# Optimization experiments

Measured on AMD Instinct MI355X. Metric: run time of the kernel, lower is better.

## Reference

```python
import jax, jax.numpy as jnp
import numpy as np

DIM = 2048
NUM_HEADS = 16
NUM_KV_HEADS = 4
HEAD_DIM = DIM // NUM_HEADS  # 128


def apply_rotary_emb(x, freqs_cis):
    # x: [b, s, h, head_dim]; freqs_cis: [s, head_dim//2, 2]
    b, s, h, d = x.shape
    xs = x.reshape(b, s, h, d // 2, 2)
    fc = freqs_cis.reshape(1, s, 1, d // 2, 2)
    real = xs[..., 0] * fc[..., 0] - xs[..., 1] * fc[..., 1]
    imag = xs[..., 1] * fc[..., 0] + xs[..., 0] * fc[..., 1]
    return jnp.stack([real, imag], axis=-1).reshape(b, s, h, d)


def setup_inputs() -> dict:
    key = jax.random.key(0)
    k1, k2, k3, k4 = jax.random.split(key, 4)
    b, s = 2, 2048
    x = jax.random.normal(k1, (b, s, DIM), dtype=jnp.float32)
    freqs_cis = jax.random.uniform(k2, (s, HEAD_DIM // 2, 2), dtype=jnp.float32)
    total_kv_dim = (NUM_HEADS + 2 * NUM_KV_HEADS) * HEAD_DIM  # 3072
    wqkv = jax.random.normal(k3, (total_kv_dim, DIM), dtype=jnp.float32) * (DIM ** -0.5)
    wo = jax.random.normal(k4, (DIM, DIM), dtype=jnp.float32) * (DIM ** -0.5)
    return {"x": x, "freqs_cis": freqs_cis, "wqkv": wqkv, "wo": wo}


def reference(x, freqs_cis, wqkv, wo):
    b, s, _ = x.shape
    kv_size = NUM_KV_HEADS * HEAD_DIM
    qkv = jnp.einsum('bsd,od->bso', x, wqkv)
    xq = qkv[..., :DIM].reshape(b, s, NUM_HEADS, HEAD_DIM)
    xk = qkv[..., DIM:DIM + kv_size].reshape(b, s, NUM_KV_HEADS, HEAD_DIM)
    xv = qkv[..., DIM + kv_size:].reshape(b, s, NUM_KV_HEADS, HEAD_DIM)
    xq = apply_rotary_emb(xq, freqs_cis)
    xk = apply_rotary_emb(xk, freqs_cis)
    # -> [b, h, s, d]
    q = xq.transpose(0, 2, 1, 3)
    k = xk.transpose(0, 2, 1, 3)
    v = xv.transpose(0, 2, 1, 3)
    rep = NUM_HEADS // NUM_KV_HEADS
    k = jnp.repeat(k, rep, axis=1)
    v = jnp.repeat(v, rep, axis=1)
    scale = HEAD_DIM ** -0.5
    scores = jnp.einsum('bhqd,bhkd->bhqk', q, k) * scale
    causal = jnp.tril(jnp.ones((s, s), dtype=bool))
    scores = jnp.where(causal[None, None], scores, jnp.finfo(scores.dtype).min)
    attn = jax.nn.softmax(scores, axis=-1)
    out = jnp.einsum('bhqk,bhkd->bhqd', attn, v)
    out = out.transpose(0, 2, 1, 3).reshape(b, s, DIM)
    return jnp.einsum('bsd,od->bso', out, wo)
```

## Files before the change

### kernel.cpp

```cpp
#include <hip/hip_runtime.h>
#include <stdint.h>

typedef uint16_t u16;
typedef float f32x4 __attribute__((ext_vector_type(4)));
typedef short bf16x8 __attribute__((ext_vector_type(8)));

constexpr int NB = 2, NS = 2048, ND = 2048, NH = 16, NKVH = 4, HDIM = 128;
constexpr int QKVD = 3072;
constexpr int TOK = NB * NS;
constexpr float SM_SCALE = 0.08838834764831845f;
constexpr float LOG2E = 1.4426950408889634f;
constexpr float QK_SCALE = SM_SCALE * LOG2E;

#define WAITVM(N) asm volatile("s_waitcnt vmcnt(" #N ")" ::: "memory")
#define WAITLGKM0 asm volatile("s_waitcnt lgkmcnt(0)" ::: "memory")
#define MEMFENCE asm volatile("" ::: "memory")

__device__ __forceinline__ u16 f2bf(float f) {
  union { float f; uint32_t u; } v; v.f = f;
  return (u16)((v.u + 0x7fffu + ((v.u >> 16) & 1u)) >> 16);
}
__device__ __forceinline__ uint32_t cvt_pk_bf16(float lo, float hi) {
  uint32_t r;
  asm("v_cvt_pk_bf16_f32 %0, %1, %2" : "=v"(r) : "v"(lo), "v"(hi));
  return r;
}

__device__ __forceinline__ void gload_lds16(const void* g, void* l) {
  void* gv = const_cast<void*>(g);
  __builtin_amdgcn_global_load_lds(
      (__attribute__((address_space(1))) void*)gv,
      (__attribute__((address_space(3))) void*)l, 16, 0, 0);
}

__global__ __launch_bounds__(256) void cvt_bf16(const float* __restrict__ src,
                                                u16* __restrict__ dst, int n4) {
  int i = blockIdx.x * 256 + threadIdx.x;
  if (i >= n4) return;
  const float4 v = reinterpret_cast<const float4*>(src)[i];
  union { u16 h[4]; uint2 u; } o;
  o.h[0] = f2bf(v.x); o.h[1] = f2bf(v.y); o.h[2] = f2bf(v.z); o.h[3] = f2bf(v.w);
  reinterpret_cast<uint2*>(dst)[i] = o.u;
}

template <int MODE>
__global__ __launch_bounds__(256, 2)
void gemm_bt(const u16* __restrict__ A, const u16* __restrict__ Bm,
             void* __restrict__ Cv, int M, int N, int K,
             const float* __restrict__ fc, u16* __restrict__ Qb,
             u16* __restrict__ Kb, u16* __restrict__ Vt) {
  __shared__ u16 As[2][128 * 32];
  __shared__ u16 Bs[2][128 * 32];
  const int tid = threadIdx.x;
  const int lane = tid & 63;
  const int wid = tid >> 6;
  const int wr = wid >> 1, wc = wid & 1;
  const int rowA0 = blockIdx.y * 128, colB0 = blockIdx.x * 128;
  const int lr = lane & 15;
  const int lg = lane >> 4;
  const int lk = lg * 8;
  const char* Ab = (const char*)A;
  const char* Bb = (const char*)Bm;
  f32x4 acc[4][4] = {};
  const int nkt = K >> 5;

  auto STAGE = [&](int kt, int buf) {
#pragma unroll
    for (int p = 0; p < 2; ++p) {
      int o = p * 4096 + tid * 16;
      int row = o >> 6, kb = o & 63;
      gload_lds16(Ab + ((size_t)(rowA0 + row) * K + kt * 32) * 2 + kb, (char*)As[buf] + o);
      gload_lds16(Bb + ((size_t)(colB0 + row) * K + kt * 32) * 2 + kb, (char*)Bs[buf] + o);
    }
  };

  STAGE(0, 0);
  for (int kt = 0; kt < nkt; ++kt) {
    const int cur = kt & 1;
    if (kt + 1 < nkt) { STAGE(kt + 1, cur ^ 1); WAITVM(4); }
    else              { WAITVM(0); }
    __builtin_amdgcn_s_barrier();
    MEMFENCE;
    const u16* Ac = As[cur];
    const u16* Bc = Bs[cur];
    bf16x8 af[4], bfr[4];
#pragma unroll
    for (int m = 0; m < 4; ++m)
      af[m] = *(const bf16x8*)&Ac[(wr * 64 + m * 16 + lr) * 32 + lk];
#pragma unroll
    for (int n = 0; n < 4; ++n)
      bfr[n] = *(const bf16x8*)&Bc[(wc * 64 + n * 16 + lr) * 32 + lk];
    __builtin_amdgcn_s_setprio(1);
#pragma unroll
    for (int m = 0; m < 4; ++m)
#pragma unroll
      for (int n = 0; n < 4; ++n)
        acc[m][n] = __builtin_amdgcn_mfma_f32_16x16x32_bf16(af[m], bfr[n], acc[m][n], 0, 0, 0);
    __builtin_amdgcn_s_setprio(0);
    WAITLGKM0;
    __builtin_amdgcn_s_barrier();
    MEMFENCE;
  }

  if (MODE == 0) {
#pragma unroll
    for (int m = 0; m < 4; ++m) {
      int row0 = rowA0 + wr * 64 + m * 16 + lg * 4;
#pragma unroll
      for (int n = 0; n < 4; ++n) {
        int col = colB0 + wc * 64 + n * 16 + lr;
#pragma unroll
        for (int r = 0; r < 4; ++r)
          ((float*)Cv)[(size_t)(row0 + r) * N + col] = acc[m][n][r];
      }
    }
  } else {
    const int colblk = colB0 >> 7;
#pragma unroll
    for (int m = 0; m < 4; ++m) {
      int row0 = rowA0 + wr * 64 + m * 16 + lg * 4;
      int b_ = row0 >> 11;
      int s0 = row0 & 2047;
#pragma unroll
      for (int n = 0; n < 4; ++n) {
        int d = wc * 64 + n * 16 + lr;
        f32x4 v = acc[m][n];
        if (colblk < 20) {
          f32x4 pw;
#pragma unroll
          for (int r = 0; r < 4; ++r) pw[r] = __shfl_xor(v[r], 1, 64);
          int p = d >> 1;
          const bool ev = !(d & 1);
#pragma unroll
          for (int r = 0; r < 4; ++r) {
            int st = s0 + r;
            float c = fc[(st * 64 + p) * 2];
            float sn = fc[(st * 64 + p) * 2 + 1];
            float res = ev ? (v[r] * c - pw[r] * sn) : (v[r] * c + pw[r] * sn);
            if (colblk < 16)
              Qb[((size_t)(b_ * NH + colblk) * NS + st) * HDIM + d] = f2bf(res);
            else
              Kb[((size_t)(b_ * NKVH + (colblk - 16)) * NS + st) * HDIM + d] =
                  f2bf(res * QK_SCALE);
          }
        } else {
          int kv = colblk - 20;
          union { u16 h[4]; uint2 u; } o;
#pragma unroll
          for (int r = 0; r < 4; ++r) o.h[r] = f2bf(v[r]);
          *(uint2*)&Vt[((size_t)(b_ * NKVH + kv) * HDIM + d) * NS + s0] = o.u;
        }
      }
    }
  }
}

__global__ __launch_bounds__(512, 2)
void flash_attn(const u16* __restrict__ Qb, const u16* __restrict__ Kb,
                const u16* __restrict__ Vt, u16* __restrict__ Ob) {
  __shared__ u16 Ks[2][64 * 128];
  __shared__ u16 Vs[2][128 * 64];
  const int idx = blockIdx.x;
  const int grp = idx & 7;
  const int b = grp >> 2, kvh = grp & 3;
  const int rest = idx >> 3;
  const int h = kvh * 4 + (rest & 3);
  const int qt = (NS / 128 - 1) - (rest >> 2);
  const int tid = threadIdx.x, lane = tid & 63, w = tid >> 6;
  const int lr = lane & 15, lg = lane >> 4;

  bf16x8 aq[4];
  {
    const u16* Qrow = Qb + ((size_t)(b * NH + h) * NS + qt * 128 + w * 16 + lr) * HDIM;
#pragma unroll
    for (int ks = 0; ks < 4; ++ks)
      aq[ks] = *(const bf16x8*)(Qrow + ks * 32 + lg * 8);
  }
  bf16x8 ones;
#pragma unroll
  for (int j = 0; j < 8; ++j) ones[j] = (short)0x3F80;

  float mrun = -1e30f;
  f32x4 accl = {0.f, 0.f, 0.f, 0.f};
  f32x4 acco[8] = {};

  const char* Kbase = (const char*)(Kb + (size_t)(b * NKVH + kvh) * NS * HDIM);
  const char* Vbase = (const char*)(Vt + (size_t)(b * NKVH + kvh) * HDIM * NS);
  const int qglob = qt * 128 + w * 16 + lr;
  const int qrow0 = qt * 128 + w * 16 + lg * 4;
  const int wave_min_row = qt * 128 + w * 16;
  const int wave_max_row = wave_min_row + 15;

  auto STAGE = [&](int kt, int buf) {
#pragma unroll
    for (int p = 0; p < 2; ++p) {
      int o = p * 8192 + tid * 16;
      int krow = o >> 8, kwb = o & 255;
      gload_lds16(Kbase + (size_t)(kt * 64 + krow) * 256 + (kwb ^ ((krow & 7) << 4)),
                  (char*)Ks[buf] + o);
      int vrow = o >> 7, vwb = o & 127;
      gload_lds16(Vbase + (size_t)vrow * (NS * 2) + kt * 128 + (vwb ^ ((vrow & 7) << 4)),
                  (char*)Vs[buf] + o);
    }
  };

  const int ktmax = 2 * qt + 1;
  STAGE(0, 0);
  for (int kt = 0; kt <= ktmax; ++kt) {
    const int cur = kt & 1;
    if (kt < ktmax) { STAGE(kt + 1, cur ^ 1); WAITVM(4); }
    else            { WAITVM(0); }
    __builtin_amdgcn_s_barrier();
    MEMFENCE;

    if (kt * 64 <= wave_max_row) {
      const char* Kc = (const char*)Ks[cur];
      const char* Vc = (const char*)Vs[cur];

      f32x4 accs[4] = {};
      __builtin_amdgcn_s_setprio(1);
#pragma unroll
      for (int n = 0; n < 4; ++n) {
        int row = n * 16 + lr;
        int swz = (row & 7) << 4;
#pragma unroll
        for (int ks = 0; ks < 4; ++ks) {
          int cb = (ks * 32 + lg * 8) * 2;
          bf16x8 bk = *(const bf16x8*)(Kc + row * 256 + (cb ^ swz));
          accs[n] = __builtin_amdgcn_mfma_f32_16x16x32_bf16(bk, aq[ks], accs[n], 0, 0, 0);
        }
      }
      __builtin_amdgcn_s_setprio(0);

      if (kt * 64 + 63 > wave_min_row) {
#pragma unroll
        for (int n = 0; n < 4; ++n) {
          int kbase = kt * 64 + n * 16 + lg * 4;
#pragma unroll
          for (int r = 0; r < 4; ++r)
            if (kbase + r > qglob) accs[n][r] = -1e30f;
        }
      }

      float pmax = fmaxf(fmaxf(fmaxf(accs[0][0], accs[0][1]), fmaxf(accs[0][2], accs[0][3])),
                         fmaxf(fmaxf(accs[1][0], accs[1][1]), fmaxf(accs[1][2], accs[1][3])));
      pmax = fmaxf(pmax,
             fmaxf(fmaxf(fmaxf(accs[2][0], accs[2][1]), fmaxf(accs[2][2], accs[2][3])),
                   fmaxf(fmaxf(accs[3][0], accs[3][1]), fmaxf(accs[3][2], accs[3][3]))));
      pmax = fmaxf(pmax, __shfl_xor(pmax, 16, 64));
      pmax = fmaxf(pmax, __shfl_xor(pmax, 32, 64));

      bool ok = (pmax <= mrun + 8.f);
      if (!__all(ok)) {
        float mnew = fmaxf(mrun, pmax);
        float alpha = exp2f(mrun - mnew);
        mrun = mnew;
        float alr[4];
#pragma unroll
        for (int r = 0; r < 4; ++r)
          alr[r] = __shfl(alpha, lg * 4 + r, 64);
#pragma unroll
        for (int r = 0; r < 4; ++r) accl[r] *= alr[r];
#pragma unroll
        for (int n2 = 0; n2 < 8; ++n2)
#pragma unroll
          for (int r = 0; r < 4; ++r) acco[n2][r] *= alr[r];
      }

      uint32_t w0[4], w1[4];
#pragma unroll
      for (int n = 0; n < 4; ++n) {
        float p0 = exp2f(accs[n][0] - mrun);
        float p1 = exp2f(accs[n][1] - mrun);
        float p2 = exp2f(accs[n][2] - mrun);
        float p3 = exp2f(accs[n][3] - mrun);
        w0[n] = cvt_pk_bf16(p0, p1);
        w1[n] = cvt_pk_bf16(p2, p3);
      }

      const int s1 = ((lg & 1) << 5) | lr;
      const int s2 = s1 + 16;
      uint32_t F[4][4];
#pragma unroll
      for (int n = 0; n < 4; ++n) {
        F[n][0] = __shfl((int)w0[n], s1, 64);
        F[n][1] = __shfl((int)w1[n], s1, 64);
        F[n][2] = __shfl((int)w0[n], s2, 64);
        F[n][3] = __shfl((int)w1[n], s2, 64);
      }
      const bool hi = (lg & 2);
      bf16x8 pa[2];
#pragma unroll
      for (int ks = 0; ks < 2; ++ks) {
        union { uint32_t d[4]; bf16x8 v; } u;
#pragma unroll
        for (int j = 0; j < 4; ++j)
          u.d[j] = hi ? F[ks * 2 + 1][j] : F[ks * 2][j];
        pa[ks] = u.v;
      }

      __builtin_amdgcn_s_setprio(1);
#pragma unroll
      for (int ks = 0; ks < 2; ++ks) {
        int cb = (ks * 32 + lg * 8) * 2;
#pragma unroll
        for (int n2 = 0; n2 < 8; ++n2) {
          int d = n2 * 16 + lr;
          bf16x8 bv = *(const bf16x8*)(Vc + d * 128 + (cb ^ ((d & 7) << 4)));
          acco[n2] = __builtin_amdgcn_mfma_f32_16x16x32_bf16(pa[ks], bv, acco[n2], 0, 0, 0);
        }
        accl = __builtin_amdgcn_mfma_f32_16x16x32_bf16(pa[ks], ones, accl, 0, 0, 0);
      }
      __builtin_amdgcn_s_setprio(0);
    }
    WAITLGKM0;
    __builtin_amdgcn_s_barrier();
    MEMFENCE;
  }

#pragma unroll
  for (int n2 = 0; n2 < 8; ++n2) {
    int d = n2 * 16 + lr;
#pragma unroll
    for (int r = 0; r < 4; ++r) {
      int q = qrow0 + r;
      Ob[((size_t)b * NS + q) * ND + h * HDIM + d] = f2bf(acco[n2][r] / accl[r]);
    }
  }
}

extern "C" void kernel_launch(void* const* d_in, const int* in_sizes, int n_in,
                              void* d_out, int out_size, void* d_ws, size_t ws_size,
                              hipStream_t stream) {
  const float* x = (const float*)d_in[0];
  const float* fc = (const float*)d_in[1];
  const float* wqkv = (const float*)d_in[2];
  const float* wo = (const float*)d_in[3];
  float* out = (float*)d_out;
  char* ws = (char*)d_ws;
  size_t off = 0;
  u16* xb = (u16*)(ws + off);    off += (size_t)TOK * ND * 2;
  u16* wqkvb = (u16*)(ws + off); off += (size_t)QKVD * ND * 2;
  u16* wob = (u16*)(ws + off);   off += (size_t)ND * ND * 2;
  u16* Qb = (u16*)(ws + off);    off += (size_t)NB * NH * NS * HDIM * 2;
  u16* Kb = (u16*)(ws + off);    off += (size_t)NB * NKVH * NS * HDIM * 2;
  u16* Vtb = (u16*)(ws + off);   off += (size_t)NB * NKVH * NS * HDIM * 2;
  u16* attnb = (u16*)(ws + off); off += (size_t)TOK * ND * 2;
  (void)ws_size; (void)in_sizes; (void)n_in; (void)out_size;

  cvt_bf16<<<TOK * ND / 4 / 256, 256, 0, stream>>>(x, xb, TOK * ND / 4);
  cvt_bf16<<<QKVD * ND / 4 / 256, 256, 0, stream>>>(wqkv, wqkvb, QKVD * ND / 4);
  cvt_bf16<<<ND * ND / 4 / 256, 256, 0, stream>>>(wo, wob, ND * ND / 4);
  gemm_bt<2><<<dim3(QKVD / 128, TOK / 128), 256, 0, stream>>>(
      xb, wqkvb, nullptr, TOK, QKVD, ND, fc, Qb, Kb, Vtb);
  flash_attn<<<dim3(NB * NKVH * (NH / NKVH) * (NS / 128)), 512, 0, stream>>>(Qb, Kb, Vtb, attnb);
  gemm_bt<0><<<dim3(ND / 128, TOK / 128), 256, 0, stream>>>(
      attnb, wob, out, TOK, ND, ND, nullptr, nullptr, nullptr, nullptr);
}
```

Measured before the change: 220.1 us.

## Give each flash-attention wave two 16-row query chunks, halving block size

The flash attention kernel now runs 4 waves of 256 threads, each covering 32 query rows as two 16-row chunks, instead of 8 waves covering 16 rows each. Every K and V fragment read from LDS now feeds two MFMAs, so LDS read traffic per FLOP is halved. Each thread now issues 4 global-to-LDS loads per stage instead of 2, and the wait count is adjusted to match. The cost is about twice the accumulator registers per wave and fewer waves per block, which may lower occupancy and latency hiding. The causal-mask wave skip is also coarser, since it now works on 32 rows.

```diff
diff --git a/kernel.cpp b/kernel.cpp
--- a/kernel.cpp
+++ b/kernel.cpp
@@ -155,7 +155,7 @@
   }
 }
 
-__global__ __launch_bounds__(512, 2)
+__global__ __launch_bounds__(256, 2)
 void flash_attn(const u16* __restrict__ Qb, const u16* __restrict__ Kb,
                 const u16* __restrict__ Vt, u16* __restrict__ Ob) {
   __shared__ u16 Ks[2][64 * 128];
@@ -169,32 +169,31 @@
   const int tid = threadIdx.x, lane = tid & 63, w = tid >> 6;
   const int lr = lane & 15, lg = lane >> 4;
 
-  bf16x8 aq[4];
-  {
-    const u16* Qrow = Qb + ((size_t)(b * NH + h) * NS + qt * 128 + w * 16 + lr) * HDIM;
+  const int wr0 = qt * 128 + w * 32;
+
+  bf16x8 aq[2][4];
+#pragma unroll
+  for (int c = 0; c < 2; ++c) {
+    const u16* Qrow = Qb + ((size_t)(b * NH + h) * NS + wr0 + c * 16 + lr) * HDIM;
 #pragma unroll
     for (int ks = 0; ks < 4; ++ks)
-      aq[ks] = *(const bf16x8*)(Qrow + ks * 32 + lg * 8);
+      aq[c][ks] = *(const bf16x8*)(Qrow + ks * 32 + lg * 8);
   }
   bf16x8 ones;
 #pragma unroll
   for (int j = 0; j < 8; ++j) ones[j] = (short)0x3F80;
 
-  float mrun = -1e30f;
-  f32x4 accl = {0.f, 0.f, 0.f, 0.f};
-  f32x4 acco[8] = {};
+  float mrun[2] = {-1e30f, -1e30f};
+  f32x4 accl[2] = {};
+  f32x4 acco[2][8] = {};
 
   const char* Kbase = (const char*)(Kb + (size_t)(b * NKVH + kvh) * NS * HDIM);
   const char* Vbase = (const char*)(Vt + (size_t)(b * NKVH + kvh) * HDIM * NS);
-  const int qglob = qt * 128 + w * 16 + lr;
-  const int qrow0 = qt * 128 + w * 16 + lg * 4;
-  const int wave_min_row = qt * 128 + w * 16;
-  const int wave_max_row = wave_min_row + 15;
 
   auto STAGE = [&](int kt, int buf) {
 #pragma unroll
-    for (int p = 0; p < 2; ++p) {
-      int o = p * 8192 + tid * 16;
+    for (int p = 0; p < 4; ++p) {
+      int o = p * 4096 + tid * 16;
       int krow = o >> 8, kwb = o & 255;
       gload_lds16(Kbase + (size_t)(kt * 64 + krow) * 256 + (kwb ^ ((krow & 7) << 4)),
                   (char*)Ks[buf] + o);
@@ -208,16 +207,16 @@
   STAGE(0, 0);
   for (int kt = 0; kt <= ktmax; ++kt) {
     const int cur = kt & 1;
-    if (kt < ktmax) { STAGE(kt + 1, cur ^ 1); WAITVM(4); }
+    if (kt < ktmax) { STAGE(kt + 1, cur ^ 1); WAITVM(8); }
     else            { WAITVM(0); }
     __builtin_amdgcn_s_barrier();
     MEMFENCE;
 
-    if (kt * 64 <= wave_max_row) {
+    if (kt * 64 <= wr0 + 31) {
       const char* Kc = (const char*)Ks[cur];
       const char* Vc = (const char*)Vs[cur];
 
-      f32x4 accs[4] = {};
+      f32x4 accs[2][4] = {};
       __builtin_amdgcn_s_setprio(1);
 #pragma unroll
       for (int n = 0; n < 4; ++n) {
@@ -227,76 +226,82 @@
         for (int ks = 0; ks < 4; ++ks) {
           int cb = (ks * 32 + lg * 8) * 2;
           bf16x8 bk = *(const bf16x8*)(Kc + row * 256 + (cb ^ swz));
-          accs[n] = __builtin_amdgcn_mfma_f32_16x16x32_bf16(bk, aq[ks], accs[n], 0, 0, 0);
+          accs[0][n] = __builtin_amdgcn_mfma_f32_16x16x32_bf16(bk, aq[0][ks], accs[0][n], 0, 0, 0);
+          accs[1][n] = __builtin_amdgcn_mfma_f32_16x16x32_bf16(bk, aq[1][ks], accs[1][n], 0, 0, 0);
         }
       }
       __builtin_amdgcn_s_setprio(0);
 
-      if (kt * 64 + 63 > wave_min_row) {
+      bf16x8 pa[2][2];
+#pragma unroll
+      for (int c = 0; c < 2; ++c) {
+        const int cmin = wr0 + c * 16;
+        const int qg = cmin + lr;
+        if (kt * 64 + 63 > cmin) {
+#pragma unroll
+          for (int n = 0; n < 4; ++n) {
+            int kbase = kt * 64 + n * 16 + lg * 4;
+#pragma unroll
+            for (int r = 0; r < 4; ++r)
+              if (kbase + r > qg) accs[c][n][r] = -1e30f;
+          }
+        }
+
+        float pmax = fmaxf(
+            fmaxf(fmaxf(fmaxf(accs[c][0][0], accs[c][0][1]), fmaxf(accs[c][0][2], accs[c][0][3])),
+                  fmaxf(fmaxf(accs[c][1][0], accs[c][1][1]), fmaxf(accs[c][1][2], accs[c][1][3]))),
+            fmaxf(fmaxf(fmaxf(accs[c][2][0], accs[c][2][1]), fmaxf(accs[c][2][2], accs[c][2][3])),
+                  fmaxf(fmaxf(accs[c][3][0], accs[c][3][1]), fmaxf(accs[c][3][2], accs[c][3][3]))));
+        pmax = fmaxf(pmax, __shfl_xor(pmax, 16, 64));
+        pmax = fmaxf(pmax, __shfl_xor(pmax, 32, 64));
+
+        bool ok = (pmax <= mrun[c] + 8.f);
+        if (!__all(ok)) {
+          float mnew = fmaxf(mrun[c], pmax);
+          float alpha = exp2f(mrun[c] - mnew);
+          mrun[c] = mnew;
+          float alr[4];
+#pragma unroll
+          for (int r = 0; r < 4; ++r)
+            alr[r] = __shfl(alpha, lg * 4 + r, 64);
+#pragma unroll
+          for (int r = 0; r < 4; ++r) accl[c][r] *= alr[r];
+#pragma unroll
+          for (int n2 = 0; n2 < 8; ++n2)
+#pragma unroll
+            for (int r = 0; r < 4; ++r) acco[c][n2][r] *= alr[r];
+        }
+
+        uint32_t w0[4], w1[4];
 #pragma unroll
         for (int n = 0; n < 4; ++n) {
-          int kbase = kt * 64 + n * 16 + lg * 4;
-#pragma unroll
-          for (int r = 0; r < 4; ++r)
-            if (kbase + r > qglob) accs[n][r] = -1e30f;
-        }
-      }
-
-      float pmax = fmaxf(fmaxf(fmaxf(accs[0][0], accs[0][1]), fmaxf(accs[0][2], accs[0][3])),
-                         fmaxf(fmaxf(accs[1][0], accs[1][1]), fmaxf(accs[1][2], accs[1][3])));
-      pmax = fmaxf(pmax,
-             fmaxf(fmaxf(fmaxf(accs[2][0], accs[2][1]), fmaxf(accs[2][2], accs[2][3])),
-                   fmaxf(fmaxf(accs[3][0], accs[3][1]), fmaxf(accs[3][2], accs[3][3]))));
-      pmax = fmaxf(pmax, __shfl_xor(pmax, 16, 64));
-      pmax = fmaxf(pmax, __shfl_xor(pmax, 32, 64));
-
-      bool ok = (pmax <= mrun + 8.f);
-      if (!__all(ok)) {
-        float mnew = fmaxf(mrun, pmax);
-        float alpha = exp2f(mrun - mnew);
-        mrun = mnew;
-        float alr[4];
-#pragma unroll
-        for (int r = 0; r < 4; ++r)
-          alr[r] = __shfl(alpha, lg * 4 + r, 64);
-#pragma unroll
-        for (int r = 0; r < 4; ++r) accl[r] *= alr[r];
-#pragma unroll
-        for (int n2 = 0; n2 < 8; ++n2)
-#pragma unroll
-          for (int r = 0; r < 4; ++r) acco[n2][r] *= alr[r];
-      }
-
-      uint32_t w0[4], w1[4];
-#pragma unroll
-      for (int n = 0; n < 4; ++n) {
-        float p0 = exp2f(accs[n][0] - mrun);
-        float p1 = exp2f(accs[n][1] - mrun);
-        float p2 = exp2f(accs[n][2] - mrun);
-        float p3 = exp2f(accs[n][3] - mrun);
-        w0[n] = cvt_pk_bf16(p0, p1);
-        w1[n] = cvt_pk_bf16(p2, p3);
-      }
-
-      const int s1 = ((lg & 1) << 5) | lr;
-      const int s2 = s1 + 16;
-      uint32_t F[4][4];
-#pragma unroll
-      for (int n = 0; n < 4; ++n) {
-        F[n][0] = __shfl((int)w0[n], s1, 64);
-        F[n][1] = __shfl((int)w1[n], s1, 64);
-        F[n][2] = __shfl((int)w0[n], s2, 64);
-        F[n][3] = __shfl((int)w1[n], s2, 64);
-      }
-      const bool hi = (lg & 2);
-      bf16x8 pa[2];
-#pragma unroll
-      for (int ks = 0; ks < 2; ++ks) {
-        union { uint32_t d[4]; bf16x8 v; } u;
-#pragma unroll
-        for (int j = 0; j < 4; ++j)
-          u.d[j] = hi ? F[ks * 2 + 1][j] : F[ks * 2][j];
-        pa[ks] = u.v;
+          float p0 = exp2f(accs[c][n][0] - mrun[c]);
+          float p1 = exp2f(accs[c][n][1] - mrun[c]);
+          float p2 = exp2f(accs[c][n][2] - mrun[c]);
+          float p3 = exp2f(accs[c][n][3] - mrun[c]);
+          w0[n] = cvt_pk_bf16(p0, p1);
+          w1[n] = cvt_pk_bf16(p2, p3);
+        }
+
+        const int s1 = ((lg & 1) << 5) | lr;
+        const int s2 = s1 + 16;
+        uint32_t F[4][4];
+#pragma unroll
+        for (int n = 0; n < 4; ++n) {
+          F[n][0] = __shfl((int)w0[n], s1, 64);
+          F[n][1] = __shfl((int)w1[n], s1, 64);
+          F[n][2] = __shfl((int)w0[n], s2, 64);
+          F[n][3] = __shfl((int)w1[n], s2, 64);
+        }
+        const bool hi = (lg & 2);
+#pragma unroll
+        for (int ks = 0; ks < 2; ++ks) {
+          union { uint32_t d[4]; bf16x8 v; } u;
+#pragma unroll
+          for (int j = 0; j < 4; ++j)
+            u.d[j] = hi ? F[ks * 2 + 1][j] : F[ks * 2][j];
+          pa[c][ks] = u.v;
+        }
       }
 
       __builtin_amdgcn_s_setprio(1);
@@ -307,9 +312,11 @@
         for (int n2 = 0; n2 < 8; ++n2) {
           int d = n2 * 16 + lr;
           bf16x8 bv = *(const bf16x8*)(Vc + d * 128 + (cb ^ ((d & 7) << 4)));
-          acco[n2] = __builtin_amdgcn_mfma_f32_16x16x32_bf16(pa[ks], bv, acco[n2], 0, 0, 0);
-        }
-        accl = __builtin_amdgcn_mfma_f32_16x16x32_bf16(pa[ks], ones, accl, 0, 0, 0);
+          acco[0][n2] = __builtin_amdgcn_mfma_f32_16x16x32_bf16(pa[0][ks], bv, acco[0][n2], 0, 0, 0);
+          acco[1][n2] = __builtin_amdgcn_mfma_f32_16x16x32_bf16(pa[1][ks], bv, acco[1][n2], 0, 0, 0);
+        }
+        accl[0] = __builtin_amdgcn_mfma_f32_16x16x32_bf16(pa[0][ks], ones, accl[0], 0, 0, 0);
+        accl[1] = __builtin_amdgcn_mfma_f32_16x16x32_bf16(pa[1][ks], ones, accl[1], 0, 0, 0);
       }
       __builtin_amdgcn_s_setprio(0);
     }
@@ -319,14 +326,16 @@
   }
 
 #pragma unroll
-  for (int n2 = 0; n2 < 8; ++n2) {
-    int d = n2 * 16 + lr;
-#pragma unroll
-    for (int r = 0; r < 4; ++r) {
-      int q = qrow0 + r;
-      Ob[((size_t)b * NS + q) * ND + h * HDIM + d] = f2bf(acco[n2][r] / accl[r]);
-    }
-  }
+  for (int c = 0; c < 2; ++c)
+#pragma unroll
+    for (int n2 = 0; n2 < 8; ++n2) {
+      int d = n2 * 16 + lr;
+#pragma unroll
+      for (int r = 0; r < 4; ++r) {
+        int q = wr0 + c * 16 + lg * 4 + r;
+        Ob[((size_t)b * NS + q) * ND + h * HDIM + d] = f2bf(acco[c][n2][r] / accl[c][r]);
+      }
+    }
 }
 
 extern "C" void kernel_launch(void* const* d_in, const int* in_sizes, int n_in,
@@ -353,7 +362,7 @@
   cvt_bf16<<<ND * ND / 4 / 256, 256, 0, stream>>>(wo, wob, ND * ND / 4);
   gemm_bt<2><<<dim3(QKVD / 128, TOK / 128), 256, 0, stream>>>(
       xb, wqkvb, nullptr, TOK, QKVD, ND, fc, Qb, Kb, Vtb);
-  flash_attn<<<dim3(NB * NKVH * (NH / NKVH) * (NS / 128)), 512, 0, stream>>>(Qb, Kb, Vtb, attnb);
+  flash_attn<<<dim3(NB * NKVH * (NH / NKVH) * (NS / 128)), 256, 0, stream>>>(Qb, Kb, Vtb, attnb);
   gemm_bt<0><<<dim3(ND / 128, TOK / 128), 256, 0, stream>>>(
       attnb, wob, out, TOK, ND, ND, nullptr, nullptr, nullptr, nullptr);
 }
```

Result: slower. 224.9 us (+2.2%).
